# Optimization experiments

Hardware: AMD Instinct MI355X
Metric: run time of the kernel (lower is better)

## Reference

```python
import jax, jax.numpy as jnp
import numpy as np

FIR = (1.0, 3.0, 3.0, 1.0)
FACTOR = 2
GAIN = 1.0


def _fir_kernel_2d():
    # _setup_kernel: 1D -> outer product, normalize, then scale by gain*factor^2
    k = np.asarray(FIR, dtype=np.float32)
    k = np.outer(k, k)
    k /= k.sum()
    return k * (GAIN * FACTOR ** 2)  # [4, 4]


def setup_inputs() -> dict:
    key = jax.random.key(0)
    kx, kw = jax.random.split(key)
    x = jax.random.normal(kx, (4, 256, 64, 64), dtype=jnp.float32)
    # DDPM variance-scaling init ~ U(-sqrt(3*var), sqrt(3*var)); plain scaled normal is fine for a numeric baseline
    w = jax.random.normal(kw, (256, 256, 3, 3), dtype=jnp.float32) * 0.02  # [outC, inC, 3, 3]
    return {"x": x, "w": w}


def reference(x, w):
    # Fused upsample(+FIR) conv: torch does conv_transpose2d(x, flip(w).permute(in,out), stride=2)
    # which is exactly a correlation of the stride-2 zero-dilated input with the ORIGINAL OIHW weight.
    N, C, H, W = x.shape
    outC, inC, kh, kw_ = w.shape
    h = jax.lax.conv_general_dilated(
        x, w,
        window_strides=(1, 1),
        padding=((kh - 1, kh - 1), (kw_ - 1, kw_ - 1)),
        lhs_dilation=(FACTOR, FACTOR),
        dimension_numbers=("NCHW", "OIHW", "NCHW"),
    )  # [N, outC, 2H+1, 2W+1]

    k = jnp.asarray(_fir_kernel_2d())  # [4,4]
    p = k.shape[0] - FACTOR - (kw_ - 1)          # = 0
    pad0 = (p + 1) // 2 + FACTOR - 1             # = 1
    pad1 = p // 2 + 1                            # = 1
    # upfirdn2d with up=1, down=1, pad=(pad0,pad1): pad then TRUE convolution (flipped kernel),
    # applied depthwise per channel.
    kflip = k[::-1, ::-1]
    kern = jnp.tile(kflip[None, None, :, :], (outC, 1, 1, 1))  # [outC, 1, 4, 4]
    out = jax.lax.conv_general_dilated(
        h, kern,
        window_strides=(1, 1),
        padding=((pad0, pad1), (pad0, pad1)),
        dimension_numbers=("NCHW", "OIHW", "NCHW"),
        feature_group_count=outC,
    )  # [N, outC, 2H, 2W]
    return out
```

## Files before the change

### kernel.cpp

```cpp
#include <hip/hip_runtime.h>
#include <hip/hip_bf16.h>


typedef short bf16x4v __attribute__((ext_vector_type(4)));
typedef short bf16x8 __attribute__((ext_vector_type(8)));
typedef short short4v __attribute__((ext_vector_type(4)));
typedef float f32x16 __attribute__((ext_vector_type(16)));
typedef float f32x4v __attribute__((ext_vector_type(4)));

static __device__ __forceinline__ short f2bf(float f) {
  __hip_bfloat16 h = __float2bfloat16(f);
  union { __hip_bfloat16 h; short s; } u; u.h = h;
  return u.s;
}
static __device__ __forceinline__ float bf2f(short s) {
  union { unsigned u; float f; } v; v.u = ((unsigned)(unsigned short)s) << 16;
  return v.f;
}

#define AS_SZ 46080
#define KQ_PLANE 5120
#define AB_OFF 2560
#define XS_BASE 92160
#define XS_SZ 14400
#define XS_STRIDE 80

__global__ __launch_bounds__(512, 2)
void fir_up_v20(const float* __restrict__ x, const float* __restrict__ w,
                float* __restrict__ out) {
  __shared__ __align__(16) char smem[120960];

  const int bid = blockIdx.x;
  const int wg = (bid & 7) * 64 + (bid >> 3);
  const int octile = wg >> 7;
  const int n = (wg >> 5) & 3;
  const int sp = wg & 31;
  const int atile = sp >> 2;
  const int btile = sp & 3;
  const int A0 = atile * 8, B0 = btile * 16;

  const int tid = threadIdx.x;
  const int wid = tid >> 6;
  const int lane = tid & 63;
  const int l31 = lane & 31, q = lane >> 5;

  const int COLSt[4]  = {17, 18, 17, 18};
  const int CELLSt[4] = {153, 162, 170, 180};
  const int NKt[4]    = {4, 2, 2, 1};
  const int KQt[4][4] = {{0,2,6,8},{1,7,7,7},{3,5,5,5},{4,4,4,4}};
  const int DYt[4][4] = {{0,0,1,1},{0,1,1,1},{0,0,0,0},{0,0,0,0}};
  const int DXt[4][4] = {{0,1,0,1},{0,0,0,0},{0,1,1,1},{0,0,0,0}};
  const int SEG0P[8]   = {0,0,0,1,1,2,2,3};
  const int SEG0FGB[8] = {0,2,4,0,3,0,3,0};
  const int SEG0NFG[8] = {2,2,1,3,3,3,3,3};

  const int p0w = SEG0P[wid];
  const int nk0 = NKt[p0w];
  const int nfg0 = SEG0NFG[wid];
  int aoff0[4];
#pragma unroll
  for (int s = 0; s < 4; ++s)
    aoff0[s] = KQt[p0w][s] * KQ_PLANE + l31 * 80 + q * 16;
  int boff0[3][4], valid0[3], hbase0[3];
#pragma unroll
  for (int fg = 0; fg < 3; ++fg) {
    const int cellraw = (SEG0FGB[wid] + fg) * 32 + l31;
    const int valid = cellraw < CELLSt[p0w];
    const int cell = valid ? cellraw : 0;
    const int cols = COLSt[p0w];
    const int r = cell / cols;
    const int c = cell - r * cols;
    valid0[fg] = valid;
    hbase0[fg] = p0w * 12800 + r * 20 + c;
#pragma unroll
    for (int s = 0; s < 4; ++s) {
      const int bc = (r + DYt[p0w][s]) * 18 + (c + DXt[p0w][s]);
      boff0[fg][s] = bc * XS_STRIDE + q * 16;
    }
  }
  const int aoff1 = 4 * KQ_PLANE + l31 * 80 + q * 16;
  int boffW0, hbaseW0;
  {
    const int cell = 96 + l31;
    const int r = cell / 18, c = cell - r * 18;
    hbaseW0 = 3 * 12800 + r * 20 + c;
    boffW0 = cell * XS_STRIDE + q * 16;
  }
  int boff1[2], valid1[2], hbase1[2];
#pragma unroll
  for (int j = 0; j < 2; ++j) {
    const int cellraw = (4 + j) * 32 + l31;
    const int valid = cellraw < 180;
    const int cell = valid ? cellraw : 0;
    const int r = cell / 18, c = cell - r * 18;
    valid1[j] = valid;
    hbase1[j] = 3 * 12800 + r * 20 + c;
    boff1[j] = cell * XS_STRIDE + q * 16;
  }

  f32x16 acc[3][2];
#pragma unroll
  for (int fg = 0; fg < 3; ++fg)
#pragma unroll
    for (int mf = 0; mf < 2; ++mf)
#pragma unroll
      for (int e = 0; e < 16; ++e) acc[fg][mf][e] = 0.f;

  const int ocA = tid >> 3, icq = tid & 7;
  const float* wA = w + (size_t)(octile * 64 + ocA) * 2304 + icq * 36;
  const int awb = ocA * 80 + icq * 8;
  int uic_[4], urow_[4], uf4g_[4], ugh_[4], ugw0_[4], uwb0_[4];
  bool uact_[4], urowok_[4], ual_[4], uint_[4];
#pragma unroll
  for (int t = 0; t < 4; ++t) {
    const int u = tid + t * 512;
    uact_[t] = u < 1920;
    const int uu = uact_[t] ? u : 0;
    uic_[t] = uu / 60;
    const int rem = uu - uic_[t] * 60;
    urow_[t] = rem / 6;
    uf4g_[t] = rem - urow_[t] * 6;
    ugh_[t] = A0 - 1 + urow_[t];
    urowok_[t] = (ugh_[t] >= 0) & (ugh_[t] < 64);
    ugw0_[t] = B0 - 4 + 4 * uf4g_[t];
    ual_[t] = (ugw0_[t] >= 0) & (ugw0_[t] <= 60);
    uint_[t] = (uf4g_[t] >= 1) & (uf4g_[t] <= 4);
    uwb0_[t] = (urow_[t] * 18 + (4 * uf4g_[t] - 3)) * XS_STRIDE + uic_[t] * 2;
  }

  {
    char* xsw = smem + XS_BASE;
#pragma unroll
    for (int t = 0; t < 4; ++t) {
      if (uact_[t]) {
        float v[4] = {0.f, 0.f, 0.f, 0.f};
        if (urowok_[t]) {
          const float* base = x + (((size_t)(n * 256 + uic_[t])) * 64 + ugh_[t]) * 64;
          if (ual_[t]) {
            const f32x4v fv = *(const f32x4v*)(base + ugw0_[t]);
#pragma unroll
            for (int e = 0; e < 4; ++e) v[e] = fv[e];
          } else {
#pragma unroll
            for (int e = 0; e < 4; ++e) {
              const int gw = ugw0_[t] + e;
              v[e] = (gw >= 0 && gw < 64) ? base[gw] : 0.f;
            }
          }
        }
        if (uint_[t]) {
#pragma unroll
          for (int e = 0; e < 4; ++e)
            *(short*)(xsw + uwb0_[t] + e * XS_STRIDE) = f2bf(v[e]);
        } else {
#pragma unroll
          for (int e = 0; e < 4; ++e) {
            const int ww = 4 * uf4g_[t] + e - 3;
            if (ww >= 0 && ww < 18)
              *(short*)(xsw + (urow_[t] * 18 + ww) * XS_STRIDE + uic_[t] * 2) = f2bf(v[e]);
          }
        }
      }
    }
    float f36[36];
#pragma unroll
    for (int j = 0; j < 9; ++j)
      *(f32x4v*)&f36[4 * j] = *(const f32x4v*)(wA + 4 * j);
#pragma unroll
    for (int kq = 0; kq < 9; ++kq) {
      bf16x4v pk;
#pragma unroll
      for (int v = 0; v < 4; ++v) pk[v] = f2bf(f36[v * 9 + kq]);
      *(bf16x4v*)(smem + kq * KQ_PLANE + awb) = pk;
    }
  }
  __syncthreads();

  for (int cc = 0; cc < 8; ++cc) {
    char* Asr = smem + (cc & 1) * AS_SZ;
    char* xsr = smem + XS_BASE + (cc & 1) * XS_SZ;
    char* Asw = smem + ((cc + 1) & 1) * AS_SZ;
    char* xsw = smem + XS_BASE + ((cc + 1) & 1) * XS_SZ;
    const bool have = cc < 7;

    float xv[4][4];
#pragma unroll
    for (int t = 0; t < 4; ++t) {
#pragma unroll
      for (int e = 0; e < 4; ++e) xv[t][e] = 0.f;
      if (have && uact_[t] && urowok_[t]) {
        const float* base =
            x + (((size_t)(n * 256 + (cc + 1) * 32 + uic_[t])) * 64 + ugh_[t]) * 64;
        if (ual_[t]) {
          const f32x4v fv = *(const f32x4v*)(base + ugw0_[t]);
#pragma unroll
          for (int e = 0; e < 4; ++e) xv[t][e] = fv[e];
        } else {
#pragma unroll
          for (int e = 0; e < 4; ++e) {
            const int gw = ugw0_[t] + e;
            xv[t][e] = (gw >= 0 && gw < 64) ? base[gw] : 0.f;
          }
        }
      }
    }
    f32x4v wv[9];
#pragma unroll
    for (int j = 0; j < 9; ++j) {
      if (have) wv[j] = *(const f32x4v*)(wA + (cc + 1) * 288 + 4 * j);
    }

    __builtin_amdgcn_s_setprio(1);
#pragma unroll
    for (int s = 0; s < 4; ++s) {
      if (s < nk0) {
#pragma unroll
        for (int h = 0; h < 2; ++h) {
          const bf16x8 Aa = *(const bf16x8*)(Asr + aoff0[s] + h * 32);
          const bf16x8 Ab = *(const bf16x8*)(Asr + aoff0[s] + h * 32 + AB_OFF);
#pragma unroll
          for (int fg = 0; fg < 3; ++fg) {
            if (fg < nfg0) {
              const bf16x8 B = *(const bf16x8*)(xsr + boff0[fg][s] + h * 32);
              acc[fg][0] = __builtin_amdgcn_mfma_f32_32x32x16_bf16(Aa, B, acc[fg][0], 0, 0, 0);
              acc[fg][1] = __builtin_amdgcn_mfma_f32_32x32x16_bf16(Ab, B, acc[fg][1], 0, 0, 0);
            }
          }
        }
      }
    }
    if (wid == 0) {
#pragma unroll
      for (int h = 0; h < 2; ++h) {
        const bf16x8 Aa = *(const bf16x8*)(Asr + aoff1 + h * 32);
        const bf16x8 Ab = *(const bf16x8*)(Asr + aoff1 + h * 32 + AB_OFF);
        const bf16x8 B = *(const bf16x8*)(xsr + boffW0 + h * 32);
        acc[2][0] = __builtin_amdgcn_mfma_f32_32x32x16_bf16(Aa, B, acc[2][0], 0, 0, 0);
        acc[2][1] = __builtin_amdgcn_mfma_f32_32x32x16_bf16(Ab, B, acc[2][1], 0, 0, 0);
      }
    }
    if (wid == 2) {
#pragma unroll
      for (int h = 0; h < 2; ++h) {
        const bf16x8 Aa = *(const bf16x8*)(Asr + aoff1 + h * 32);
        const bf16x8 Ab = *(const bf16x8*)(Asr + aoff1 + h * 32 + AB_OFF);
#pragma unroll
        for (int j = 0; j < 2; ++j) {
          const bf16x8 B = *(const bf16x8*)(xsr + boff1[j] + h * 32);
          acc[1 + j][0] = __builtin_amdgcn_mfma_f32_32x32x16_bf16(Aa, B, acc[1 + j][0], 0, 0, 0);
          acc[1 + j][1] = __builtin_amdgcn_mfma_f32_32x32x16_bf16(Ab, B, acc[1 + j][1], 0, 0, 0);
        }
      }
    }
    __builtin_amdgcn_s_setprio(0);

    if (have) {
#pragma unroll
      for (int t = 0; t < 4; ++t) {
        if (uact_[t]) {
          if (uint_[t]) {
#pragma unroll
            for (int e = 0; e < 4; ++e)
              *(short*)(xsw + uwb0_[t] + e * XS_STRIDE) = f2bf(xv[t][e]);
          } else {
#pragma unroll
            for (int e = 0; e < 4; ++e) {
              const int ww = 4 * uf4g_[t] + e - 3;
              if (ww >= 0 && ww < 18)
                *(short*)(xsw + (urow_[t] * 18 + ww) * XS_STRIDE + uic_[t] * 2) = f2bf(xv[t][e]);
            }
          }
        }
      }
#pragma unroll
      for (int kq = 0; kq < 9; ++kq) {
        bf16x4v pk;
#pragma unroll
        for (int v = 0; v < 4; ++v) {
          const int flat = v * 9 + kq;
          pk[v] = f2bf(wv[flat >> 2][flat & 3]);
        }
        *(bf16x4v*)(Asw + kq * KQ_PLANE + awb) = pk;
      }
    }
    __syncthreads();
  }

  short* hl = (short*)smem;
  const float kf4[4] = {0.25f, 0.75f, 0.75f, 0.25f};
#pragma unroll
  for (int fg = 0; fg < 3; ++fg) {
    if (fg < nfg0 && valid0[fg]) {
#pragma unroll
      for (int mf = 0; mf < 2; ++mf)
#pragma unroll
        for (int e = 0; e < 16; ++e) {
          const int ocl = (e & 3) + 8 * (e >> 2) + 4 * q + 32 * mf;
          hl[hbase0[fg] + ocl * 200] = f2bf(acc[fg][mf][e]);
        }
    }
  }
  if (wid == 0) {
#pragma unroll
    for (int mf = 0; mf < 2; ++mf)
#pragma unroll
      for (int e = 0; e < 16; ++e) {
        const int ocl = (e & 3) + 8 * (e >> 2) + 4 * q + 32 * mf;
        hl[hbaseW0 + ocl * 200] = f2bf(acc[2][mf][e]);
      }
  }
  if (wid == 2) {
#pragma unroll
    for (int j = 0; j < 2; ++j) {
      if (valid1[j]) {
#pragma unroll
        for (int mf = 0; mf < 2; ++mf)
#pragma unroll
          for (int e = 0; e < 16; ++e) {
            const int ocl = (e & 3) + 8 * (e >> 2) + 4 * q + 32 * mf;
            hl[hbase1[j] + ocl * 200] = f2bf(acc[1 + j][mf][e]);
          }
      }
    }
  }
  __syncthreads();
#pragma unroll
  for (int k = 0; k < 8; ++k) {
    const int v = tid + k * 512;
    const int g = v & 3;
    const int Yl = (v >> 2) & 15;
    const int ocl = v >> 6;
    float o[8];
#pragma unroll
    for (int xx = 0; xx < 8; ++xx) o[xx] = 0.f;
#pragma unroll
    for (int du = 0; du < 4; ++du) {
      const int ttp = Yl - 1 + du;
      const int py = ttp & 1;
      const int r = py ? ((Yl + du) >> 1) : (ttp >> 1);
      const int baseE = (py * 2) * 12800 + ocl * 200 + r * 20 + 4 * g;
      const int baseO = baseE + 12800;
      const short4v e0 = *(const short4v*)(hl + baseE);
      const short4v e1 = *(const short4v*)(hl + baseE + 4);
      const short4v o0 = *(const short4v*)(hl + baseO);
      const short4v o1 = *(const short4v*)(hl + baseO + 4);
      float E[8], O[8];
#pragma unroll
      for (int i = 0; i < 4; ++i) {
        E[i] = bf2f(e0[i]); E[i + 4] = bf2f(e1[i]);
        O[i] = bf2f(o0[i]); O[i + 4] = bf2f(o1[i]);
      }
      float rx[8];
      rx[0] = 0.25f*O[0] + 0.75f*E[0] + 0.75f*O[1] + 0.25f*E[1];
      rx[1] = 0.25f*E[0] + 0.75f*O[1] + 0.75f*E[1] + 0.25f*O[2];
      rx[2] = 0.25f*O[1] + 0.75f*E[1] + 0.75f*O[2] + 0.25f*E[2];
      rx[3] = 0.25f*E[1] + 0.75f*O[2] + 0.75f*E[2] + 0.25f*O[3];
      rx[4] = 0.25f*O[2] + 0.75f*E[2] + 0.75f*O[3] + 0.25f*E[3];
      rx[5] = 0.25f*E[2] + 0.75f*O[3] + 0.75f*E[3] + 0.25f*O[4];
      rx[6] = 0.25f*O[3] + 0.75f*E[3] + 0.75f*O[4] + 0.25f*E[4];
      rx[7] = 0.25f*E[3] + 0.75f*O[4] + 0.75f*E[4] + 0.25f*O[5];
      const float ky = kf4[du];
#pragma unroll
      for (int xx = 0; xx < 8; ++xx) o[xx] += ky * rx[xx];
    }
    const int oc = octile * 64 + ocl;
    const int Y = atile * 16 + Yl;
    const int X0 = btile * 32 + g * 8;
    float* op = out + (((size_t)(n * 256 + oc)) * 128 + Y) * 128 + X0;
    f32x4v v0, v1;
    v0[0] = o[0]; v0[1] = o[1]; v0[2] = o[2]; v0[3] = o[3];
    v1[0] = o[4]; v1[1] = o[5]; v1[2] = o[6]; v1[3] = o[7];
    *(f32x4v*)op = v0;
    *(f32x4v*)(op + 4) = v1;
  }
}

extern "C" void kernel_launch(void* const* d_in, const int* in_sizes, int n_in,
                              void* d_out, int out_size, void* d_ws, size_t ws_size,
                              hipStream_t stream) {
  (void)in_sizes; (void)n_in; (void)out_size; (void)d_ws; (void)ws_size;
  const float* x = (const float*)d_in[0];
  const float* w = (const float*)d_in[1];
  float* out = (float*)d_out;
  hipLaunchKernelGGL(fir_up_v20, dim3(512), dim3(512), 0, stream, x, w, out);
}
```

Measured before the change: 81.70 us.

## Prefetch input two chunks ahead and pack channel pairs into 32-bit LDS stores

The input-tile staging now has each thread load two adjacent channels and write them to LDS as one packed 32-bit store instead of separate 16-bit stores. The x global loads are issued two chunks ahead using two register buffers in a manually unrolled ping-pong loop. Weight loads move into the staging step after the MFMA block, so they are no longer prefetched across it. The aim is fewer LDS store instructions and more global-load latency hidden behind MFMA work, at the cost of more live registers, which could hurt occupancy at launch bounds 512,2.

```diff
diff --git a/kernel.cpp b/kernel.cpp
--- a/kernel.cpp
+++ b/kernel.cpp
@@ -16,6 +16,9 @@
 static __device__ __forceinline__ float bf2f(short s) {
   union { unsigned u; float f; } v; v.u = ((unsigned)(unsigned short)s) << 16;
   return v.f;
+}
+static __device__ __forceinline__ int pack2(float a, float b) {
+  return ((int)(unsigned short)f2bf(a)) | (((int)(unsigned short)f2bf(b)) << 16);
 }
 
 #define AS_SZ 46080
@@ -26,7 +29,7 @@
 #define XS_STRIDE 80
 
 __global__ __launch_bounds__(512, 2)
-void fir_up_v20(const float* __restrict__ x, const float* __restrict__ w,
+void fir_up_v21(const float* __restrict__ x, const float* __restrict__ w,
                 float* __restrict__ out) {
   __shared__ __align__(16) char smem[120960];
 
@@ -109,15 +112,15 @@
   const int ocA = tid >> 3, icq = tid & 7;
   const float* wA = w + (size_t)(octile * 64 + ocA) * 2304 + icq * 36;
   const int awb = ocA * 80 + icq * 8;
-  int uic_[4], urow_[4], uf4g_[4], ugh_[4], ugw0_[4], uwb0_[4];
-  bool uact_[4], urowok_[4], ual_[4], uint_[4];
-#pragma unroll
-  for (int t = 0; t < 4; ++t) {
+  int uicp_[2], urow_[2], uf4g_[2], ugh_[2], ugw0_[2], uwb0_[2];
+  bool uact_[2], urowok_[2], ual_[2], uint_[2];
+#pragma unroll
+  for (int t = 0; t < 2; ++t) {
     const int u = tid + t * 512;
-    uact_[t] = u < 1920;
+    uact_[t] = u < 960;
     const int uu = uact_[t] ? u : 0;
-    uic_[t] = uu / 60;
-    const int rem = uu - uic_[t] * 60;
+    uicp_[t] = uu / 60;
+    const int rem = uu - uicp_[t] * 60;
     urow_[t] = rem / 6;
     uf4g_[t] = rem - urow_[t] * 6;
     ugh_[t] = A0 - 1 + urow_[t];
@@ -125,165 +128,145 @@
     ugw0_[t] = B0 - 4 + 4 * uf4g_[t];
     ual_[t] = (ugw0_[t] >= 0) & (ugw0_[t] <= 60);
     uint_[t] = (uf4g_[t] >= 1) & (uf4g_[t] <= 4);
-    uwb0_[t] = (urow_[t] * 18 + (4 * uf4g_[t] - 3)) * XS_STRIDE + uic_[t] * 2;
-  }
+    uwb0_[t] = (urow_[t] * 18 + (4 * uf4g_[t] - 3)) * XS_STRIDE + uicp_[t] * 4;
+  }
+
+#define LOAD_X(xv, CH)                                                         \
+  {                                                                            \
+    _Pragma("unroll") for (int t = 0; t < 2; ++t) {                            \
+      _Pragma("unroll") for (int j = 0; j < 8; ++j) xv[t][j] = 0.f;            \
+      if (uact_[t] && urowok_[t]) {                                            \
+        const float* baseA =                                                   \
+            x + (((size_t)(n * 256 + (CH) * 32 + 2 * uicp_[t])) * 64 + ugh_[t]) * 64; \
+        if (ual_[t]) {                                                         \
+          const f32x4v fA = *(const f32x4v*)(baseA + ugw0_[t]);                \
+          const f32x4v fB = *(const f32x4v*)(baseA + 4096 + ugw0_[t]);         \
+          _Pragma("unroll") for (int e = 0; e < 4; ++e) {                      \
+            xv[t][e] = fA[e]; xv[t][4 + e] = fB[e];                            \
+          }                                                                    \
+        } else {                                                               \
+          _Pragma("unroll") for (int e = 0; e < 4; ++e) {                      \
+            const int gw = ugw0_[t] + e;                                       \
+            const bool ok = (gw >= 0) & (gw < 64);                             \
+            xv[t][e] = ok ? baseA[gw] : 0.f;                                   \
+            xv[t][4 + e] = ok ? baseA[4096 + gw] : 0.f;                        \
+          }                                                                    \
+        }                                                                      \
+      }                                                                        \
+    }                                                                          \
+  }
+
+#define WRITE_X(XSW, xv)                                                       \
+  {                                                                            \
+    _Pragma("unroll") for (int t = 0; t < 2; ++t) {                            \
+      if (uact_[t]) {                                                          \
+        if (uint_[t]) {                                                        \
+          _Pragma("unroll") for (int e = 0; e < 4; ++e)                        \
+            *(int*)((XSW) + uwb0_[t] + e * XS_STRIDE) =                        \
+                pack2(xv[t][e], xv[t][4 + e]);                                 \
+        } else {                                                               \
+          _Pragma("unroll") for (int e = 0; e < 4; ++e) {                      \
+            const int ww = 4 * uf4g_[t] + e - 3;                               \
+            if (ww >= 0 && ww < 18)                                            \
+              *(int*)((XSW) + (urow_[t] * 18 + ww) * XS_STRIDE + uicp_[t] * 4) = \
+                  pack2(xv[t][e], xv[t][4 + e]);                               \
+          }                                                                    \
+        }                                                                      \
+      }                                                                        \
+    }                                                                          \
+  }
+
+#define MFMA_CHUNK(ASR, XSR)                                                   \
+  {                                                                            \
+    __builtin_amdgcn_s_setprio(1);                                             \
+    _Pragma("unroll") for (int s = 0; s < 4; ++s) {                            \
+      if (s < nk0) {                                                           \
+        _Pragma("unroll") for (int h = 0; h < 2; ++h) {                        \
+          const bf16x8 Aa = *(const bf16x8*)((ASR) + aoff0[s] + h * 32);       \
+          const bf16x8 Ab = *(const bf16x8*)((ASR) + aoff0[s] + h * 32 + AB_OFF); \
+          _Pragma("unroll") for (int fg = 0; fg < 3; ++fg) {                   \
+            if (fg < nfg0) {                                                   \
+              const bf16x8 B = *(const bf16x8*)((XSR) + boff0[fg][s] + h * 32);\
+              acc[fg][0] = __builtin_amdgcn_mfma_f32_32x32x16_bf16(Aa, B, acc[fg][0], 0, 0, 0); \
+              acc[fg][1] = __builtin_amdgcn_mfma_f32_32x32x16_bf16(Ab, B, acc[fg][1], 0, 0, 0); \
+            }                                                                  \
+          }                                                                    \
+        }                                                                      \
+      }                                                                        \
+    }                                                                          \
+    if (wid == 0) {                                                            \
+      _Pragma("unroll") for (int h = 0; h < 2; ++h) {                          \
+        const bf16x8 Aa = *(const bf16x8*)((ASR) + aoff1 + h * 32);            \
+        const bf16x8 Ab = *(const bf16x8*)((ASR) + aoff1 + h * 32 + AB_OFF);   \
+        const bf16x8 B = *(const bf16x8*)((XSR) + boffW0 + h * 32);            \
+        acc[2][0] = __builtin_amdgcn_mfma_f32_32x32x16_bf16(Aa, B, acc[2][0], 0, 0, 0); \
+        acc[2][1] = __builtin_amdgcn_mfma_f32_32x32x16_bf16(Ab, B, acc[2][1], 0, 0, 0); \
+      }                                                                        \
+    }                                                                          \
+    if (wid == 2) {                                                            \
+      _Pragma("unroll") for (int h = 0; h < 2; ++h) {                          \
+        const bf16x8 Aa = *(const bf16x8*)((ASR) + aoff1 + h * 32);            \
+        const bf16x8 Ab = *(const bf16x8*)((ASR) + aoff1 + h * 32 + AB_OFF);   \
+        _Pragma("unroll") for (int j = 0; j < 2; ++j) {                        \
+          const bf16x8 B = *(const bf16x8*)((XSR) + boff1[j] + h * 32);        \
+          acc[1 + j][0] = __builtin_amdgcn_mfma_f32_32x32x16_bf16(Aa, B, acc[1 + j][0], 0, 0, 0); \
+          acc[1 + j][1] = __builtin_amdgcn_mfma_f32_32x32x16_bf16(Ab, B, acc[1 + j][1], 0, 0, 0); \
+        }                                                                      \
+      }                                                                        \
+    }                                                                          \
+    __builtin_amdgcn_s_setprio(0);                                             \
+  }
+
+#define STAGE_W(ASW, CH)                                                       \
+  {                                                                            \
+    f32x4v wv[9];                                                              \
+    _Pragma("unroll") for (int j = 0; j < 9; ++j)                              \
+      wv[j] = *(const f32x4v*)(wA + (CH) * 288 + 4 * j);                       \
+    _Pragma("unroll") for (int kq = 0; kq < 9; ++kq) {                         \
+      bf16x4v pk;                                                              \
+      _Pragma("unroll") for (int v = 0; v < 4; ++v) {                          \
+        const int flat = v * 9 + kq;                                           \
+        pk[v] = f2bf(wv[flat >> 2][flat & 3]);                                 \
+      }                                                                        \
+      *(bf16x4v*)((ASW) + kq * KQ_PLANE + awb) = pk;                           \
+    }                                                                          \
+  }
+
+  float xvA[2][8], xvB[2][8];
 
   {
-    char* xsw = smem + XS_BASE;
-#pragma unroll
-    for (int t = 0; t < 4; ++t) {
-      if (uact_[t]) {
-        float v[4] = {0.f, 0.f, 0.f, 0.f};
-        if (urowok_[t]) {
-          const float* base = x + (((size_t)(n * 256 + uic_[t])) * 64 + ugh_[t]) * 64;
-          if (ual_[t]) {
-            const f32x4v fv = *(const f32x4v*)(base + ugw0_[t]);
-#pragma unroll
-            for (int e = 0; e < 4; ++e) v[e] = fv[e];
-          } else {
-#pragma unroll
-            for (int e = 0; e < 4; ++e) {
-              const int gw = ugw0_[t] + e;
-              v[e] = (gw >= 0 && gw < 64) ? base[gw] : 0.f;
-            }
-          }
-        }
-        if (uint_[t]) {
-#pragma unroll
-          for (int e = 0; e < 4; ++e)
-            *(short*)(xsw + uwb0_[t] + e * XS_STRIDE) = f2bf(v[e]);
-        } else {
-#pragma unroll
-          for (int e = 0; e < 4; ++e) {
-            const int ww = 4 * uf4g_[t] + e - 3;
-            if (ww >= 0 && ww < 18)
-              *(short*)(xsw + (urow_[t] * 18 + ww) * XS_STRIDE + uic_[t] * 2) = f2bf(v[e]);
-          }
-        }
-      }
-    }
-    float f36[36];
-#pragma unroll
-    for (int j = 0; j < 9; ++j)
-      *(f32x4v*)&f36[4 * j] = *(const f32x4v*)(wA + 4 * j);
-#pragma unroll
-    for (int kq = 0; kq < 9; ++kq) {
-      bf16x4v pk;
-#pragma unroll
-      for (int v = 0; v < 4; ++v) pk[v] = f2bf(f36[v * 9 + kq]);
-      *(bf16x4v*)(smem + kq * KQ_PLANE + awb) = pk;
-    }
+    LOAD_X(xvB, 0);
+    WRITE_X(smem + XS_BASE, xvB);
+    STAGE_W(smem, 0);
+    LOAD_X(xvA, 1);
   }
   __syncthreads();
 
-  for (int cc = 0; cc < 8; ++cc) {
-    char* Asr = smem + (cc & 1) * AS_SZ;
-    char* xsr = smem + XS_BASE + (cc & 1) * XS_SZ;
-    char* Asw = smem + ((cc + 1) & 1) * AS_SZ;
-    char* xsw = smem + XS_BASE + ((cc + 1) & 1) * XS_SZ;
-    const bool have = cc < 7;
-
-    float xv[4][4];
-#pragma unroll
-    for (int t = 0; t < 4; ++t) {
-#pragma unroll
-      for (int e = 0; e < 4; ++e) xv[t][e] = 0.f;
-      if (have && uact_[t] && urowok_[t]) {
-        const float* base =
-            x + (((size_t)(n * 256 + (cc + 1) * 32 + uic_[t])) * 64 + ugh_[t]) * 64;
-        if (ual_[t]) {
-          const f32x4v fv = *(const f32x4v*)(base + ugw0_[t]);
-#pragma unroll
-          for (int e = 0; e < 4; ++e) xv[t][e] = fv[e];
-        } else {
-#pragma unroll
-          for (int e = 0; e < 4; ++e) {
-            const int gw = ugw0_[t] + e;
-            xv[t][e] = (gw >= 0 && gw < 64) ? base[gw] : 0.f;
-          }
-        }
-      }
-    }
-    f32x4v wv[9];
-#pragma unroll
-    for (int j = 0; j < 9; ++j) {
-      if (have) wv[j] = *(const f32x4v*)(wA + (cc + 1) * 288 + 4 * j);
-    }
-
-    __builtin_amdgcn_s_setprio(1);
-#pragma unroll
-    for (int s = 0; s < 4; ++s) {
-      if (s < nk0) {
-#pragma unroll
-        for (int h = 0; h < 2; ++h) {
-          const bf16x8 Aa = *(const bf16x8*)(Asr + aoff0[s] + h * 32);
-          const bf16x8 Ab = *(const bf16x8*)(Asr + aoff0[s] + h * 32 + AB_OFF);
-#pragma unroll
-          for (int fg = 0; fg < 3; ++fg) {
-            if (fg < nfg0) {
-              const bf16x8 B = *(const bf16x8*)(xsr + boff0[fg][s] + h * 32);
-              acc[fg][0] = __builtin_amdgcn_mfma_f32_32x32x16_bf16(Aa, B, acc[fg][0], 0, 0, 0);
-              acc[fg][1] = __builtin_amdgcn_mfma_f32_32x32x16_bf16(Ab, B, acc[fg][1], 0, 0, 0);
-            }
-          }
-        }
-      }
-    }
-    if (wid == 0) {
-#pragma unroll
-      for (int h = 0; h < 2; ++h) {
-        const bf16x8 Aa = *(const bf16x8*)(Asr + aoff1 + h * 32);
-        const bf16x8 Ab = *(const bf16x8*)(Asr + aoff1 + h * 32 + AB_OFF);
-        const bf16x8 B = *(const bf16x8*)(xsr + boffW0 + h * 32);
-        acc[2][0] = __builtin_amdgcn_mfma_f32_32x32x16_bf16(Aa, B, acc[2][0], 0, 0, 0);
-        acc[2][1] = __builtin_amdgcn_mfma_f32_32x32x16_bf16(Ab, B, acc[2][1], 0, 0, 0);
-      }
-    }
-    if (wid == 2) {
-#pragma unroll
-      for (int h = 0; h < 2; ++h) {
-        const bf16x8 Aa = *(const bf16x8*)(Asr + aoff1 + h * 32);
-        const bf16x8 Ab = *(const bf16x8*)(Asr + aoff1 + h * 32 + AB_OFF);
-#pragma unroll
-        for (int j = 0; j < 2; ++j) {
-          const bf16x8 B = *(const bf16x8*)(xsr + boff1[j] + h * 32);
-          acc[1 + j][0] = __builtin_amdgcn_mfma_f32_32x32x16_bf16(Aa, B, acc[1 + j][0], 0, 0, 0);
-          acc[1 + j][1] = __builtin_amdgcn_mfma_f32_32x32x16_bf16(Ab, B, acc[1 + j][1], 0, 0, 0);
-        }
-      }
-    }
-    __builtin_amdgcn_s_setprio(0);
-
-    if (have) {
-#pragma unroll
-      for (int t = 0; t < 4; ++t) {
-        if (uact_[t]) {
-          if (uint_[t]) {
-#pragma unroll
-            for (int e = 0; e < 4; ++e)
-              *(short*)(xsw + uwb0_[t] + e * XS_STRIDE) = f2bf(xv[t][e]);
-          } else {
-#pragma unroll
-            for (int e = 0; e < 4; ++e) {
-              const int ww = 4 * uf4g_[t] + e - 3;
-              if (ww >= 0 && ww < 18)
-                *(short*)(xsw + (urow_[t] * 18 + ww) * XS_STRIDE + uic_[t] * 2) = f2bf(xv[t][e]);
-            }
-          }
-        }
-      }
-#pragma unroll
-      for (int kq = 0; kq < 9; ++kq) {
-        bf16x4v pk;
-#pragma unroll
-        for (int v = 0; v < 4; ++v) {
-          const int flat = v * 9 + kq;
-          pk[v] = f2bf(wv[flat >> 2][flat & 3]);
-        }
-        *(bf16x4v*)(Asw + kq * KQ_PLANE + awb) = pk;
-      }
-    }
-    __syncthreads();
+  char* As0 = smem;
+  char* As1 = smem + AS_SZ;
+  char* xs0 = smem + XS_BASE;
+  char* xs1 = smem + XS_BASE + XS_SZ;
+  for (int ccp = 0; ccp < 4; ++ccp) {
+    const int cc0 = 2 * ccp;
+    {
+      if (cc0 + 2 <= 7) LOAD_X(xvB, cc0 + 2);
+      MFMA_CHUNK(As0, xs0);
+      if (cc0 + 1 <= 7) {
+        WRITE_X(xs1, xvA);
+        STAGE_W(As1, cc0 + 1);
+      }
+      __syncthreads();
+    }
+    const int cc1 = cc0 + 1;
+    {
+      if (cc1 + 2 <= 7) LOAD_X(xvA, cc1 + 2);
+      MFMA_CHUNK(As1, xs1);
+      if (cc1 + 1 <= 7) {
+        WRITE_X(xs0, xvB);
+        STAGE_W(As0, cc1 + 1);
+      }
+      __syncthreads();
+    }
   }
 
   short* hl = (short*)smem;
@@ -382,5 +365,5 @@
   const float* x = (const float*)d_in[0];
   const float* w = (const float*)d_in[1];
   float* out = (float*)d_out;
-  hipLaunchKernelGGL(fir_up_v20, dim3(512), dim3(512), 0, stream, x, w, out);
-}
+  hipLaunchKernelGGL(fir_up_v21, dim3(512), dim3(512), 0, stream, x, w, out);
+}
```

Result: faster. 73.65 us (-9.9%).
